# Optimization experiments

Hardware: AMD Instinct MI355X
Metric: run time of the kernel (lower is better)

Reference implementation:

```python
import jax, jax.numpy as jnp
import numpy as np

NUM_EMBED = 204
HEAD_DIM = 64
B, T = 4, 4096


def setup_inputs() -> dict:
    key = jax.random.key(0)
    kx, kq, kk, kv = jax.random.split(key, 4)
    x = jax.random.normal(kx, (B, T, NUM_EMBED), dtype=jnp.float32)
    s = 1.0 / np.sqrt(NUM_EMBED)
    Wq = jax.random.normal(kq, (NUM_EMBED, HEAD_DIM), dtype=jnp.float32) * s
    Wk = jax.random.normal(kk, (NUM_EMBED, HEAD_DIM), dtype=jnp.float32) * s
    Wv = jax.random.normal(kv, (NUM_EMBED, HEAD_DIM), dtype=jnp.float32) * s
    return {"x": x, "Wq": Wq, "Wk": Wk, "Wv": Wv, "mask": True}


def reference(x, Wq, Wk, Wv, mask):
    # Single-head causal attention. d_k = x.shape[-1] (as in the source, which
    # scales by sqrt of the INPUT embed dim, not head_dim).
    Bn, Tn, d_k = x.shape
    q = x @ Wq  # [B,T,H]
    k = x @ Wk  # [B,T,H]
    v = x @ Wv  # [B,T,H]
    scale = 1.0 / jnp.sqrt(jnp.asarray(d_k, dtype=x.dtype))
    scores = jnp.einsum("bqh,bkh->bqk", q, k) * scale  # [B,T,T]
    if mask:
        causal = jnp.tril(jnp.ones((Tn, Tn), dtype=bool))  # allow j <= i
        scores = jnp.where(causal, scores, jnp.finfo(scores.dtype).min)
    attn = jax.nn.softmax(scores, axis=-1)
    out = jnp.einsum("bqk,bkh->bqh", attn, v)  # [B,T,H]
    # dropout is identity in eval mode
    return out
```

## Files before the change

kernel.cpp:

```cpp
#include <hip/hip_runtime.h>

#define TSEQ   4096
#define NB     4
#define EMB    204
#define HD     64
#define WK     224
#define XSTR   232
#define KSTR   72
#define VSTR   136
#define PSTR   68
#define BIG_NEG (-3.0e38f)

typedef __attribute__((ext_vector_type(8))) short bf16x8;
typedef __attribute__((ext_vector_type(4))) float f32x4;

__device__ __forceinline__ short f2bf(float f) {
    unsigned u = __float_as_uint(f);
    return (short)((u + 0x7fffu + ((u >> 16) & 1u)) >> 16);
}
__device__ __forceinline__ float bf2f(short h) {
    return __uint_as_float(((unsigned)(unsigned short)h) << 16);
}

__global__ __launch_bounds__(256) void prep_zero_kernel(
    const float* __restrict__ Wq,
    const float* __restrict__ Wk,
    const float* __restrict__ Wv,
    short* __restrict__ Wt,
    float* __restrict__ zacc)
{
    int f = blockIdx.x * 256 + threadIdx.x;
    if (f < 3 * HD * WK) {
        int e   = f % WK;
        int h   = (f / WK) % HD;
        int mat = f / (WK * HD);
        const float* W = (mat == 0) ? Wq : (mat == 1) ? Wk : Wv;
        float v = (e < EMB) ? W[e * HD + h] : 0.f;
        Wt[f] = f2bf(v);
    }
    for (int c = blockIdx.x * 256 + threadIdx.x; c < 266240; c += 256 * 256)
        *(float4*)(zacc + c * 4) = make_float4(0.f, 0.f, 0.f, 0.f);
}

__global__ __launch_bounds__(192) void qkv_mfma_kernel(
    const float* __restrict__ x,
    const short* __restrict__ Wt,
    short* __restrict__ qg,
    short* __restrict__ kg,
    short* __restrict__ vtg)
{
    __shared__ __align__(16) short xs[16 * XSTR];

    const int t    = threadIdx.x;
    const int lane = t & 63;
    const int w    = t >> 6;
    const int l15  = lane & 15;
    const int quad = lane >> 4;
    const long long rowb = (long long)blockIdx.x * 16;

    for (int c = t; c < 816; c += 192) {
        int r = c / 51, c4 = c % 51;
        float4 xv = *(const float4*)(x + (rowb + r) * EMB + c4 * 4);
        unsigned p0 = (unsigned)(unsigned short)f2bf(xv.x)
                    | ((unsigned)(unsigned short)f2bf(xv.y) << 16);
        unsigned p1 = (unsigned)(unsigned short)f2bf(xv.z)
                    | ((unsigned)(unsigned short)f2bf(xv.w) << 16);
        uint2 pk; pk.x = p0; pk.y = p1;
        *(uint2*)(&xs[r * XSTR + c4 * 4]) = pk;
    }
    for (int c = t; c < 16 * 28; c += 192) {
        int r = c / 28, cc = c % 28;
        xs[r * XSTR + EMB + cc] = 0;
    }
    __syncthreads();

    f32x4 acc[4];
#pragma unroll
    for (int nt = 0; nt < 4; ++nt) acc[nt] = (f32x4){0.f, 0.f, 0.f, 0.f};

    const short* Wb = Wt + (size_t)w * HD * WK;
#pragma unroll
    for (int ks = 0; ks < 7; ++ks) {
        bf16x8 af = *(const bf16x8*)(&xs[l15 * XSTR + ks * 32 + quad * 8]);
#pragma unroll
        for (int nt = 0; nt < 4; ++nt) {
            bf16x8 bfr = *(const bf16x8*)(Wb + (size_t)(nt * 16 + l15) * WK
                                          + ks * 32 + quad * 8);
            acc[nt] = __builtin_amdgcn_mfma_f32_16x16x32_bf16(af, bfr, acc[nt], 0, 0, 0);
        }
    }

    const float scale = 0.07001400420f;
    if (w == 0) {
#pragma unroll
        for (int r = 0; r < 4; ++r) {
            long long grow = rowb + quad * 4 + r;
#pragma unroll
            for (int nt = 0; nt < 4; ++nt)
                qg[grow * HD + nt * 16 + l15] = f2bf(acc[nt][r] * scale);
        }
    } else if (w == 1) {
#pragma unroll
        for (int r = 0; r < 4; ++r) {
            long long grow = rowb + quad * 4 + r;
#pragma unroll
            for (int nt = 0; nt < 4; ++nt)
                kg[grow * HD + nt * 16 + l15] = f2bf(acc[nt][r]);
        }
    } else {
#pragma unroll
        for (int r = 0; r < 4; ++r) {
            long long grow = rowb + quad * 4 + r;
            int bb = (int)(grow >> 12);
            int tt = (int)(grow & 4095);
#pragma unroll
            for (int nt = 0; nt < 4; ++nt)
                vtg[((long long)bb * HD + nt * 16 + l15) * TSEQ + tt] = f2bf(acc[nt][r]);
        }
    }
}

__global__ __launch_bounds__(256) void flash_mfma_kernel(
    const short* __restrict__ qg,
    const short* __restrict__ kg,
    const short* __restrict__ vtg,
    float* __restrict__ outacc,
    float* __restrict__ lacc)
{
    __shared__ __align__(16) short Ks[128 * KSTR];
    __shared__ __align__(16) short Vt[HD * VSTR];
    __shared__ __align__(16) short Ps[4 * 16 * PSTR];

    const int t    = threadIdx.x;
    const int lane = t & 63;
    const int w    = t >> 6;
    const int pair = w & 1;
    const int par  = w >> 1;
    const int l15  = lane & 15;
    const int quad = lane >> 4;

    const int b = blockIdx.y;
    const int p = 319 - (int)blockIdx.x;

    int a, idx, s;
    if (p < 32)       { a = p >> 2;                idx = p & 3;           s = 1; }
    else if (p < 96)  { a = 8 + ((p - 32) >> 3);   idx = (p - 32) & 7;    s = 2; }
    else if (p < 192) { a = 16 + (p - 96) / 12;    idx = (p - 96) % 12;   s = 3; }
    else              { a = 24 + ((p - 192) >> 4); idx = (p - 192) & 15;  s = 4; }
    const int qt    = 4 * a + idx / s;
    const int split = idx % s;
    const int ntiles = a + 1;
    const int chunk  = (ntiles + s - 1) / s;
    const int kt0    = split * chunk;
    const int kt1    = min(ntiles, kt0 + chunk);

    const int qbase = qt * 32;
    const long long rowb = (long long)b * TSEQ;

    bf16x8 aq[2];
#pragma unroll
    for (int ss = 0; ss < 2; ++ss)
        aq[ss] = *(const bf16x8*)(qg + (rowb + qbase + pair * 16 + l15) * HD
                                  + ss * 32 + quad * 8);

    f32x4 Oacc[4];
#pragma unroll
    for (int nt = 0; nt < 4; ++nt) Oacc[nt] = (f32x4){0.f, 0.f, 0.f, 0.f};
    float lsum[4] = {0.f, 0.f, 0.f, 0.f};

    short* pw = &Ps[w * 16 * PSTR];

    for (int kt = kt0; kt < kt1; ++kt) {
        const int k0 = kt * 128;
        const bool masked = (kt == ntiles - 1);
        __syncthreads();

#pragma unroll
        for (int i = 0; i < 4; ++i) {
            int c = t + i * 256;
            int r = c >> 3, c8 = (c & 7) * 8;
            *(int4*)(&Ks[r * KSTR + c8]) =
                *(const int4*)(kg + (rowb + k0 + r) * HD + c8);
        }
#pragma unroll
        for (int i = 0; i < 4; ++i) {
            int c = t + i * 256;
            int r = c >> 4, c8 = (c & 15) * 8;
            *(int4*)(&Vt[r * VSTR + c8]) =
                *(const int4*)(vtg + ((long long)b * HD + r) * TSEQ + k0 + c8);
        }
        __syncthreads();

        f32x4 S[4];
#pragma unroll
        for (int nt = 0; nt < 4; ++nt) S[nt] = (f32x4){0.f, 0.f, 0.f, 0.f};
#pragma unroll
        for (int ss = 0; ss < 2; ++ss) {
#pragma unroll
            for (int nt = 0; nt < 4; ++nt) {
                bf16x8 bk = *(const bf16x8*)(&Ks[(par * 64 + nt * 16 + l15) * KSTR
                                                 + ss * 32 + quad * 8]);
                S[nt] = __builtin_amdgcn_mfma_f32_16x16x32_bf16(aq[ss], bk, S[nt], 0, 0, 0);
            }
        }

        if (!masked) {
#pragma unroll
            for (int r = 0; r < 4; ++r) {
#pragma unroll
                for (int nt = 0; nt < 4; ++nt) {
                    float pv = __expf(S[nt][r]);
                    short h = f2bf(pv);
                    pw[(quad * 4 + r) * PSTR + nt * 16 + l15] = h;
                    lsum[r] += bf2f(h);
                }
            }
        } else {
#pragma unroll
            for (int r = 0; r < 4; ++r) {
                const int irow = qbase + pair * 16 + quad * 4 + r;
#pragma unroll
                for (int nt = 0; nt < 4; ++nt) {
                    int j = k0 + par * 64 + nt * 16 + l15;
                    float pv = (j <= irow) ? __expf(S[nt][r]) : 0.f;
                    short h = f2bf(pv);
                    pw[(quad * 4 + r) * PSTR + nt * 16 + l15] = h;
                    lsum[r] += bf2f(h);
                }
            }
        }

#pragma unroll
        for (int ss = 0; ss < 2; ++ss) {
            bf16x8 pa = *(const bf16x8*)(&pw[l15 * PSTR + ss * 32 + quad * 8]);
#pragma unroll
            for (int nt = 0; nt < 4; ++nt) {
                bf16x8 vb = *(const bf16x8*)(&Vt[(nt * 16 + l15) * VSTR
                                                 + par * 64 + ss * 32 + quad * 8]);
                Oacc[nt] = __builtin_amdgcn_mfma_f32_16x16x32_bf16(pa, vb, Oacc[nt], 0, 0, 0);
            }
        }
    }

#pragma unroll
    for (int r = 0; r < 4; ++r) {
#pragma unroll
        for (int off = 1; off < 16; off <<= 1)
            lsum[r] += __shfl_xor(lsum[r], off, 64);
    }

    float* oa = outacc + (rowb + qbase + pair * 16) * HD;
#pragma unroll
    for (int r = 0; r < 4; ++r) {
        int row = quad * 4 + r;
#pragma unroll
        for (int nt = 0; nt < 4; ++nt)
            atomicAdd(&oa[row * HD + nt * 16 + l15], Oacc[nt][r]);
        if (l15 == 0)
            atomicAdd(&lacc[rowb + qbase + pair * 16 + row], lsum[r]);
    }
}

__global__ __launch_bounds__(256) void finalize_kernel(
    const float* __restrict__ outacc,
    const float* __restrict__ lacc,
    float* __restrict__ out)
{
    int row = blockIdx.x * 16 + (threadIdx.x >> 4);
    int c4  = (threadIdx.x & 15) * 4;
    float inv = 1.0f / lacc[row];
    float4 v = *(const float4*)(outacc + (size_t)row * HD + c4);
    v.x *= inv; v.y *= inv; v.z *= inv; v.w *= inv;
    *(float4*)(out + (size_t)row * HD + c4) = v;
}

extern "C" void kernel_launch(void* const* d_in, const int* in_sizes, int n_in,
                              void* d_out, int out_size, void* d_ws, size_t ws_size,
                              hipStream_t stream)
{
    const float* x  = (const float*)d_in[0];
    const float* Wq = (const float*)d_in[1];
    const float* Wk = (const float*)d_in[2];
    const float* Wv = (const float*)d_in[3];

    const size_t nrows = (size_t)NB * TSEQ;
    short* qg  = (short*)d_ws;
    short* kg  = qg + nrows * HD;
    short* vtg = kg + nrows * HD;
    short* Wt  = vtg + nrows * HD;
    float* outacc = (float*)(Wt + 3 * HD * WK);
    float* lacc   = outacc + nrows * HD;
    float* outp = (float*)d_out;

    prep_zero_kernel<<<dim3(256), dim3(256), 0, stream>>>(Wq, Wk, Wv, Wt, outacc);
    qkv_mfma_kernel<<<dim3(1024), dim3(192), 0, stream>>>(x, Wt, qg, kg, vtg);
    flash_mfma_kernel<<<dim3(320, NB), dim3(256), 0, stream>>>(qg, kg, vtg, outacc, lacc);
    finalize_kernel<<<dim3(1024), dim3(256), 0, stream>>>(outacc, lacc, outp);
}
```

Baseline: 126.1 us.

## Load K and V MFMA fragments directly from global memory, drop LDS staging

Removes the shared-memory staging of K and V tiles along with the two block-wide barriers per key tile. Each wave now reads its MFMA B-operand fragments straight from global memory (through the L1/L2 caches). The aim is to cut LDS traffic and barrier stalls and to lower LDS use so more blocks fit per CU. In exchange, each wave issues redundant global loads, since K is read by both query-pair waves and V by both wave pairs, and global-load latency is now exposed without explicit prefetching.

```diff
diff --git a/kernel.cpp b/kernel.cpp
--- a/kernel.cpp
+++ b/kernel.cpp
@@ -6,8 +6,6 @@
 #define HD     64
 #define WK     224
 #define XSTR   232
-#define KSTR   72
-#define VSTR   136
 #define PSTR   68
 #define BIG_NEG (-3.0e38f)
 
@@ -127,8 +125,6 @@
     float* __restrict__ outacc,
     float* __restrict__ lacc)
 {
-    __shared__ __align__(16) short Ks[128 * KSTR];
-    __shared__ __align__(16) short Vt[HD * VSTR];
     __shared__ __align__(16) short Ps[4 * 16 * PSTR];
 
     const int t    = threadIdx.x;
@@ -170,26 +166,13 @@
 
     short* pw = &Ps[w * 16 * PSTR];
 
+    const short* kfrag = kg + (rowb + par * 64 + l15) * HD + quad * 8;
+    const short* vfrag = vtg + ((long long)b * HD + l15) * TSEQ
+                       + par * 64 + quad * 8;
+
     for (int kt = kt0; kt < kt1; ++kt) {
         const int k0 = kt * 128;
         const bool masked = (kt == ntiles - 1);
-        __syncthreads();
-
-#pragma unroll
-        for (int i = 0; i < 4; ++i) {
-            int c = t + i * 256;
-            int r = c >> 3, c8 = (c & 7) * 8;
-            *(int4*)(&Ks[r * KSTR + c8]) =
-                *(const int4*)(kg + (rowb + k0 + r) * HD + c8);
-        }
-#pragma unroll
-        for (int i = 0; i < 4; ++i) {
-            int c = t + i * 256;
-            int r = c >> 4, c8 = (c & 15) * 8;
-            *(int4*)(&Vt[r * VSTR + c8]) =
-                *(const int4*)(vtg + ((long long)b * HD + r) * TSEQ + k0 + c8);
-        }
-        __syncthreads();
 
         f32x4 S[4];
 #pragma unroll
@@ -198,8 +181,8 @@
         for (int ss = 0; ss < 2; ++ss) {
 #pragma unroll
             for (int nt = 0; nt < 4; ++nt) {
-                bf16x8 bk = *(const bf16x8*)(&Ks[(par * 64 + nt * 16 + l15) * KSTR
-                                                 + ss * 32 + quad * 8]);
+                bf16x8 bk = *(const bf16x8*)(kfrag + (size_t)(k0 + nt * 16) * HD
+                                             + ss * 32);
                 S[nt] = __builtin_amdgcn_mfma_f32_16x16x32_bf16(aq[ss], bk, S[nt], 0, 0, 0);
             }
         }
@@ -235,8 +218,8 @@
             bf16x8 pa = *(const bf16x8*)(&pw[l15 * PSTR + ss * 32 + quad * 8]);
 #pragma unroll
             for (int nt = 0; nt < 4; ++nt) {
-                bf16x8 vb = *(const bf16x8*)(&Vt[(nt * 16 + l15) * VSTR
-                                                 + par * 64 + ss * 32 + quad * 8]);
+                bf16x8 vb = *(const bf16x8*)(vfrag + (size_t)(nt * 16) * TSEQ
+                                             + k0 + ss * 32);
                 Oacc[nt] = __builtin_amdgcn_mfma_f32_16x16x32_bf16(pa, vb, Oacc[nt], 0, 0, 0);
             }
         }
```

Result: slower. 170.5 us (+35.3%).
